# Kernel tuning notes

Hardware: AMD Instinct MI355X
Metric: run time of the kernel (lower is better)

## Reference

```python
import jax, jax.numpy as jnp
import numpy as np

DIN = 512      # input feature dim (din)
HEADS = 8
DHEAD = 64
DIM = HEADS * DHEAD  # 512
NTOT = 12288   # total nodes across all graphs
NBATCH = 32    # number of graphs
NMAX = 512     # padded max nodes per graph (<= pf_threshold ~562 -> softmax branch)
EPS = 1e-5


def setup_inputs() -> dict:
    key = jax.random.key(0)
    ks = jax.random.split(key, 7)
    z = jax.random.normal(ks[0], (NTOT, DIN), jnp.float32)
    src = jnp.sort(jax.random.randint(ks[1], (NTOT,), 0, NBATCH)).astype(jnp.int32)
    w_scale = 1.0 / np.sqrt(DIN)
    Wq = jax.random.normal(ks[2], (DIN, DIM), jnp.float32) * w_scale
    Wk = jax.random.normal(ks[3], (DIN, DIM), jnp.float32) * w_scale
    Wv = jax.random.normal(ks[4], (DIN, DIM), jnp.float32) * w_scale
    Wo = jax.random.normal(ks[5], (DIM, DIM), jnp.float32) * w_scale
    bo = jnp.zeros((DIM,), jnp.float32)
    ln_gamma = jnp.ones((DIN,), jnp.float32)
    ln_beta = jnp.zeros((DIN,), jnp.float32)
    return {"z": z, "src": src, "ln_gamma": ln_gamma, "ln_beta": ln_beta,
            "Wq": Wq, "Wk": Wk, "Wv": Wv, "Wo": Wo, "bo": bo,
            "n_max": NMAX, "n_batch": NBATCH}


def reference(z, src, ln_gamma, ln_beta, Wq, Wk, Wv, Wo, bo, n_max, n_batch):
    # --- LayerNorm(din) ---
    mu = jnp.mean(z, axis=-1, keepdims=True)
    var = jnp.mean(jnp.square(z - mu), axis=-1, keepdims=True)
    zn = (z - mu) * jax.lax.rsqrt(var + EPS) * ln_gamma + ln_beta

    # --- to_dense_batch(zn, src): src is sorted graph-id per node ---
    ntot = z.shape[0]
    counts = jnp.bincount(src, length=n_batch)                    # [B]
    starts = jnp.concatenate([jnp.zeros((1,), counts.dtype), jnp.cumsum(counts)[:-1]])
    pos = jnp.arange(ntot) - starts[src]                          # position within graph
    x = jnp.zeros((n_batch, n_max, DIN), zn.dtype).at[src, pos].set(zn)   # [B,N,din]
    mask = jnp.zeros((n_batch, n_max), bool).at[src, pos].set(True)       # [B,N]

    # --- q/k/v projections, split heads: b n (h d) -> b h n d ---
    def heads(t):
        return t.reshape(n_batch, n_max, HEADS, DHEAD).transpose(0, 2, 1, 3)
    q = heads(x @ Wq)
    k = heads(x @ Wk)
    v = heads(x @ Wv)

    # --- manual masked softmax attention (N <= pf_threshold branch) ---
    s = jnp.einsum('bhmd,bhnd->bhmn', q, k)
    s = jnp.where(mask[:, None, None, :], s, -jnp.inf)
    a = jax.nn.softmax(s * (DHEAD ** -0.5), axis=-1)
    o = jnp.einsum('bhmn,bhnd->bhmd', a, v)

    # --- merge heads, gather valid rows (out[mask]), output projection ---
    o = o.transpose(0, 2, 1, 3).reshape(n_batch, n_max, DIM)
    h = o[src, pos] @ Wo + bo                                     # [Ntot, DIM]
    return h
```

## Files before the change

### kernel.cpp

```cpp
#include <hip/hip_runtime.h>
#include <hip/hip_bf16.h>
#include <math.h>

#define DIN 512
#define DIM 512
#define NHEADS 8
#define DHEAD 64
#define NB 32
#define NPAD 512
#define NPTOT (NB * NPAD)

typedef __attribute__((ext_vector_type(8))) short bf16x8;
typedef __attribute__((ext_vector_type(8))) unsigned short u16x8;
typedef __attribute__((ext_vector_type(4))) float f32x4;

typedef __attribute__((address_space(3))) unsigned int lds_u32;
typedef __attribute__((address_space(1))) const unsigned int g_u32;

__device__ __forceinline__ void gll16(const unsigned short* g, unsigned short* l) {
  __builtin_amdgcn_global_load_lds((g_u32*)g, (lds_u32*)l, 16, 0, 0);
}

__device__ inline unsigned short f2bf(float x) {
  unsigned int u = __float_as_uint(x);
  unsigned int r = (u + 0x7FFFu + ((u >> 16) & 1u)) >> 16;
  return (unsigned short)r;
}

#define BAR()   __builtin_amdgcn_s_barrier()
#define LGKM0() asm volatile("s_waitcnt lgkmcnt(0)" ::: "memory")
#define LGKM8() asm volatile("s_waitcnt lgkmcnt(8)" ::: "memory")
#define VMCNT(n) asm volatile("s_waitcnt vmcnt(" #n ")" ::: "memory")

__global__ __launch_bounds__(256) void prep_kernel(const float* __restrict__ z,
                                                   const float* __restrict__ gamma,
                                                   const float* __restrict__ beta,
                                                   const int* __restrict__ src,
                                                   const float* __restrict__ Wq,
                                                   const float* __restrict__ Wk,
                                                   const float* __restrict__ Wv,
                                                   const float* __restrict__ Wo,
                                                   unsigned short* __restrict__ zn,
                                                   int* __restrict__ starts,
                                                   int* __restrict__ dstrow,
                                                   unsigned short* __restrict__ WtQKV,
                                                   unsigned short* __restrict__ WtO,
                                                   int ntot) {
  __shared__ float tile[32][33];
  int b = blockIdx.x;
  int nln = ntot >> 2;
  int nmap = (ntot + 255) >> 8;
  if (b < nln) {
    int wave = b * 4 + (threadIdx.x >> 6);
    int lane = threadIdx.x & 63;
    const float* row = z + (size_t)wave * DIN;
    float4 a = ((const float4*)row)[lane];
    float4 bb = ((const float4*)row)[64 + lane];
    float s  = a.x + a.y + a.z + a.w + bb.x + bb.y + bb.z + bb.w;
    float sq = a.x*a.x + a.y*a.y + a.z*a.z + a.w*a.w
             + bb.x*bb.x + bb.y*bb.y + bb.z*bb.z + bb.w*bb.w;
#pragma unroll
    for (int off = 32; off; off >>= 1) {
      s  += __shfl_xor(s, off);
      sq += __shfl_xor(sq, off);
    }
    float mu  = s * (1.0f / DIN);
    float var = sq * (1.0f / DIN) - mu * mu;
    float r   = rsqrtf(var + 1e-5f);
    float4 g0 = ((const float4*)gamma)[lane];
    float4 g1 = ((const float4*)gamma)[64 + lane];
    float4 b0 = ((const float4*)beta)[lane];
    float4 b1 = ((const float4*)beta)[64 + lane];
    ushort4 o0, o1;
    o0.x = f2bf((a.x - mu) * r * g0.x + b0.x);
    o0.y = f2bf((a.y - mu) * r * g0.y + b0.y);
    o0.z = f2bf((a.z - mu) * r * g0.z + b0.z);
    o0.w = f2bf((a.w - mu) * r * g0.w + b0.w);
    o1.x = f2bf((bb.x - mu) * r * g1.x + b1.x);
    o1.y = f2bf((bb.y - mu) * r * g1.y + b1.y);
    o1.z = f2bf((bb.z - mu) * r * g1.z + b1.z);
    o1.w = f2bf((bb.w - mu) * r * g1.w + b1.w);
    ((ushort4*)(zn + (size_t)wave * DIN))[lane] = o0;
    ((ushort4*)(zn + (size_t)wave * DIN))[64 + lane] = o1;
  } else if (b < nln + nmap) {
    int bid = b - nln;
    if (bid == 0 && threadIdx.x <= NB) {
      int gg = threadIdx.x;
      int lo = 0, hi = ntot;
      while (lo < hi) { int mid = (lo + hi) >> 1; if (src[mid] < gg) lo = mid + 1; else hi = mid; }
      starts[gg] = lo;
    }
    int i = bid * 256 + threadIdx.x;
    if (i < ntot) {
      int gg = src[i];
      int lo = 0, hi = ntot;
      while (lo < hi) { int mid = (lo + hi) >> 1; if (src[mid] < gg) lo = mid + 1; else hi = mid; }
      dstrow[i] = gg * NPAD + (i - lo);
    }
  } else {
    int idx = b - nln - nmap;
    int zz = idx >> 8;
    int rem = idx & 255;
    const float* W; unsigned short* Wt;
    if (zz == 0)      { W = Wq; Wt = WtQKV; }
    else if (zz == 1) { W = Wk; Wt = WtQKV + (size_t)512 * DIN; }
    else if (zz == 2) { W = Wv; Wt = WtQKV + (size_t)1024 * DIN; }
    else              { W = Wo; Wt = WtO; }
    int k0 = (rem & 15) * 32;
    int n0 = (rem >> 4) * 32;
    int tx = threadIdx.x & 31;
    int ty = threadIdx.x >> 5;
#pragma unroll
    for (int i = 0; i < 4; i++)
      tile[ty + i * 8][tx] = W[(size_t)(k0 + ty + i * 8) * DIM + n0 + tx];
    __syncthreads();
#pragma unroll
    for (int i = 0; i < 4; i++)
      Wt[(size_t)(n0 + ty + i * 8) * DIN + k0 + tx] = f2bf(tile[tx][ty + i * 8]);
  }
}

__global__ __launch_bounds__(512) void gemm_qkv_8ph(const unsigned short* __restrict__ A,
                                                    const unsigned short* __restrict__ Bt,
                                                    const int* __restrict__ remap,
                                                    unsigned short* __restrict__ C) {
  __shared__ unsigned short smem[65536];
  const int tid = threadIdx.x;
  const int lane = tid & 63, wv = tid >> 6;
  const int wr = wv >> 2, wc = wv & 3;
  const int col16 = lane & 15, quad = lane >> 4;
  const int m0 = blockIdx.x * 256, n0 = blockIdx.y * 256;

  f32x4 acc[2][2][4][2];
#pragma unroll
  for (int qa = 0; qa < 2; ++qa)
#pragma unroll
    for (int qb = 0; qb < 2; ++qb)
#pragma unroll
      for (int mt = 0; mt < 4; ++mt)
#pragma unroll
        for (int nt = 0; nt < 2; ++nt) acc[qa][qb][mt][nt] = (f32x4){0.f, 0.f, 0.f, 0.f};

  bf16x8 af[4][2], bf[2][2];

  auto stage = [&](int par, int w, const unsigned short* G, int row0, int kt) {
    unsigned short* base = smem + par * 32768 + w * 8192;
#pragma unroll
    for (int i = 0; i < 2; ++i) {
      int c1k = wv * 2 + i;
      int r = row0 + c1k * 8 + (lane >> 3);
      int p = (lane & 7) ^ (lane >> 3);
      gll16(G + (size_t)r * 512 + kt * 64 + p * 8, base + c1k * 512);
    }
  };
  auto loadA = [&](int par, int half) {
    const unsigned short* base = smem + par * 32768 + half * 8192;
#pragma unroll
    for (int mt = 0; mt < 4; ++mt) {
      int r = wr * 64 + mt * 16 + col16;
      int sw = r & 7;
      af[mt][0] = *(const bf16x8*)&base[r * 64 + ((quad ^ sw) * 8)];
      af[mt][1] = *(const bf16x8*)&base[r * 64 + (((quad + 4) ^ sw) * 8)];
    }
  };
  auto loadB = [&](int par, int half) {
    const unsigned short* base = smem + par * 32768 + (2 + half) * 8192;
#pragma unroll
    for (int nt = 0; nt < 2; ++nt) {
      int r = wc * 32 + nt * 16 + col16;
      int sw = r & 7;
      bf[nt][0] = *(const bf16x8*)&base[r * 64 + ((quad ^ sw) * 8)];
      bf[nt][1] = *(const bf16x8*)&base[r * 64 + (((quad + 4) ^ sw) * 8)];
    }
  };
  auto mfmaQ = [&](int qa, int qb) {
    __builtin_amdgcn_s_setprio(1);
#pragma unroll
    for (int mt = 0; mt < 4; ++mt)
#pragma unroll
      for (int nt = 0; nt < 2; ++nt) {
        acc[qa][qb][mt][nt] =
            __builtin_amdgcn_mfma_f32_16x16x32_bf16(af[mt][0], bf[nt][0], acc[qa][qb][mt][nt], 0, 0, 0);
        acc[qa][qb][mt][nt] =
            __builtin_amdgcn_mfma_f32_16x16x32_bf16(af[mt][1], bf[nt][1], acc[qa][qb][mt][nt], 0, 0, 0);
      }
    __builtin_amdgcn_s_setprio(0);
  };

  stage(0, 0, A,  m0,       0);
  stage(0, 3, Bt, n0 + 128, 0);
  stage(0, 1, A,  m0 + 128, 0);
  stage(0, 2, Bt, n0,       0);
  stage(1, 0, A,  m0,       1);
  stage(1, 3, Bt, n0 + 128, 1);
  VMCNT(4);
  BAR();

#pragma unroll
  for (int i = 0; i < 4; ++i) {
    const int t1 = 2 * i + 1, t2 = 2 * i + 2, t3 = 2 * i + 3;
    const bool more = (i < 3);
    loadA(0, 0); loadB(0, 0);
    stage(1, 1, A, m0 + 128, t1);
    LGKM8();
    BAR(); LGKM0();
    mfmaQ(0, 0);
    BAR();
    loadB(0, 1);
    stage(1, 2, Bt, n0, t1);
    BAR(); LGKM0();
    mfmaQ(0, 1);
    BAR();
    loadA(0, 1);
    if (more) stage(0, 0, A, m0, t2);
    BAR(); LGKM0();
    mfmaQ(1, 1);
    BAR();
    loadB(0, 0);
    if (more) stage(0, 3, Bt, n0 + 128, t2);
    BAR(); LGKM0();
    mfmaQ(1, 0);
    if (more) { VMCNT(4); } else { VMCNT(0); }
    BAR();
    loadA(1, 0); loadB(1, 0);
    if (more) stage(0, 1, A, m0 + 128, t2);
    LGKM8();
    BAR(); LGKM0();
    mfmaQ(0, 0);
    BAR();
    loadB(1, 1);
    if (more) stage(0, 2, Bt, n0, t2);
    BAR(); LGKM0();
    mfmaQ(0, 1);
    BAR();
    loadA(1, 1);
    if (more) stage(1, 0, A, m0, t3);
    BAR(); LGKM0();
    mfmaQ(1, 1);
    BAR();
    loadB(1, 0);
    if (more) stage(1, 3, Bt, n0 + 128, t3);
    BAR(); LGKM0();
    mfmaQ(1, 0);
    if (more) VMCNT(4);
    BAR();
  }

#pragma unroll
  for (int qa = 0; qa < 2; ++qa)
#pragma unroll
    for (int qb = 0; qb < 2; ++qb)
#pragma unroll
      for (int mt = 0; mt < 4; ++mt)
#pragma unroll
        for (int nt = 0; nt < 2; ++nt)
#pragma unroll
          for (int r = 0; r < 4; ++r) {
            int row = qa * 128 + wr * 64 + mt * 16 + quad * 4 + r;
            int c   = qb * 128 + wc * 32 + nt * 16 + col16;
            smem[row * 256 + (((c >> 3) ^ (row & 31)) * 8) + (c & 7)] = f2bf(acc[qa][qb][mt][nt][r]);
          }
  __syncthreads();
#pragma unroll
  for (int pass = 0; pass < 16; ++pass) {
    int row = pass * 16 + (tid >> 5);
    int ch  = tid & 31;
    u16x8 v = *(const u16x8*)&smem[row * 256 + ((ch ^ (row & 31)) * 8)];
    int drow = remap[m0 + row];
    *(u16x8*)(C + (size_t)drow * 1536 + n0 + ch * 8) = v;
  }
}

template <int NCOLS, bool BIAS, bool OUT_F32, bool REMAP>
__global__ __launch_bounds__(256) void gemm_staged(const unsigned short* __restrict__ A,
                                                   const unsigned short* __restrict__ Bt,
                                                   const float* __restrict__ bias,
                                                   const int* __restrict__ remap,
                                                   unsigned short* __restrict__ Cbf,
                                                   float* __restrict__ Cf) {
  __shared__ unsigned short smem[16384];
  int tid = threadIdx.x, lane = tid & 63, wv = tid >> 6;
  int col = lane & 15, quad = lane >> 4;
  int m0 = blockIdx.x * 128, n0 = blockIdx.y * 128;
  int msub = (wv & 1) * 64, nsub = (wv >> 1) * 64;

  int srow = lane >> 2;
  int cswz = (((lane & 3) ^ ((lane >> 3) & 3))) * 8;

  f32x4 acc[4][4];
#pragma unroll
  for (int i = 0; i < 4; i++)
#pragma unroll
    for (int j = 0; j < 4; j++) acc[i][j] = (f32x4){0.f, 0.f, 0.f, 0.f};

  auto stage = [&](int ks, int nb) {
    const unsigned short* Ab = A  + (size_t)m0 * DIN + ks * 32;
    const unsigned short* Bb = Bt + (size_t)n0 * DIN + ks * 32;
#pragma unroll
    for (int i = 0; i < 2; i++) {
      int t = wv * 2 + i;
      gll16(Ab + (size_t)(t * 16 + srow) * DIN + cswz, smem + nb * 4096 + t * 512);
      gll16(Bb + (size_t)(t * 16 + srow) * DIN + cswz, smem + 8192 + nb * 4096 + t * 512);
    }
  };

  stage(0, 0);
#pragma unroll 2
  for (int ks = 0; ks < 16; ks++) {
    int cur = ks & 1;
    __syncthreads();
    if (ks + 1 < 16) stage(ks + 1, 1 - cur);
    bf16x8 af[4], bfr[4];
#pragma unroll
    for (int mt = 0; mt < 4; mt++) {
      int row = msub + mt * 16 + col;
      af[mt] = *(const bf16x8*)&smem[cur * 4096 + row * 32 + ((quad ^ ((row >> 1) & 3)) * 8)];
    }
#pragma unroll
    for (int nt = 0; nt < 4; nt++) {
      int row = nsub + nt * 16 + col;
      bfr[nt] = *(const bf16x8*)&smem[8192 + cur * 4096 + row * 32 + ((quad ^ ((row >> 1) & 3)) * 8)];
    }
#pragma unroll
    for (int mt = 0; mt < 4; mt++)
#pragma unroll
      for (int nt = 0; nt < 4; nt++)
        acc[mt][nt] = __builtin_amdgcn_mfma_f32_16x16x32_bf16(af[mt], bfr[nt], acc[mt][nt], 0, 0, 0);
  }

  if (!OUT_F32) {
    __syncthreads();
#pragma unroll
    for (int mt = 0; mt < 4; mt++)
#pragma unroll
      for (int r = 0; r < 4; r++) {
        int row = msub + mt * 16 + quad * 4 + r;
#pragma unroll
        for (int nt = 0; nt < 4; nt++) {
          int c = nsub + nt * 16 + col;
          float v = acc[mt][nt][r] + (BIAS ? bias[n0 + c] : 0.f);
          smem[row * 128 + (((c >> 3) ^ (quad << 1)) * 8) + (c & 7)] = f2bf(v);
        }
      }
    __syncthreads();
#pragma unroll
    for (int pass = 0; pass < 8; pass++) {
      int row = pass * 16 + (tid >> 4);
      int sw  = ((row >> 2) & 3) << 1;
      int ch  = tid & 15;
      u16x8 vv = *(const u16x8*)&smem[row * 128 + ((ch ^ sw) * 8)];
      int drow = REMAP ? remap[m0 + row] : (m0 + row);
      *(u16x8*)(Cbf + (size_t)drow * NCOLS + n0 + ch * 8) = vv;
    }
  } else {
#pragma unroll
    for (int mt = 0; mt < 4; mt++) {
#pragma unroll
      for (int r = 0; r < 4; r++) {
        int mrow = m0 + msub + mt * 16 + quad * 4 + r;
#pragma unroll
        for (int nt = 0; nt < 4; nt++) {
          int ncol = n0 + nsub + nt * 16 + col;
          Cf[(size_t)mrow * NCOLS + ncol] = acc[mt][nt][r] + (BIAS ? bias[ncol] : 0.f);
        }
      }
    }
  }
}

__global__ __launch_bounds__(256, 3) void fattn_kernel(const unsigned short* __restrict__ qkvp,
                                                       const int* __restrict__ starts,
                                                       unsigned short* __restrict__ obuf) {
  __shared__ unsigned short Kbuf[2][64 * 64];
  __shared__ unsigned short Vbuf[2][64 * 64];
  __shared__ unsigned short Plds[4][32 * 64];
  int g = blockIdx.x, h = blockIdx.y, qt = blockIdx.z;
  int st = starts[g];
  int n  = starts[g + 1] - st;
  int q0b = qt * 128;
  if (q0b >= n) return;
  int tid = threadIdx.x, lane = tid & 63, wv = tid >> 6;
  int col = lane & 15, quad = lane >> 4;
  int q0 = q0b + wv * 32;
  bool active = q0 < n;
  int ntiles = (n + 63) >> 6;

  bf16x8 qf[2][2];
  if (active) {
#pragma unroll
    for (int a = 0; a < 2; a++) {
      const unsigned short* qp = qkvp + (size_t)(g * NPAD + q0 + a * 16 + col) * 1536 + h * 64 + quad * 8;
      qf[a][0] = *(const bf16x8*)(qp);
      qf[a][1] = *(const bf16x8*)(qp + 32);
    }
  }

  int srow = tid >> 2;
  int sc   = (tid & 3) * 2;
  int woff0 = srow * 64 + ((sc ^ (srow & 7)) * 8);
  int woff1 = srow * 64 + (((sc + 1) ^ (srow & 7)) * 8);
  u16x8 kreg0, kreg1, vreg0, vreg1;
  auto loadregs = [&](int kt) {
    const unsigned short* kp = qkvp + (size_t)(g * NPAD + kt + srow) * 1536 + 512 + h * 64 + sc * 8;
    kreg0 = *(const u16x8*)(kp);
    kreg1 = *(const u16x8*)(kp + 8);
    vreg0 = *(const u16x8*)(kp + 512);
    vreg1 = *(const u16x8*)(kp + 520);
  };
  auto writelds = [&](int bsel) {
    *(u16x8*)&Kbuf[bsel][woff0] = kreg0;
    *(u16x8*)&Kbuf[bsel][woff1] = kreg1;
#pragma unroll
    for (int i = 0; i < 8; i++) {
      int c0 = sc * 8 + i;
      int c1 = sc * 8 + 8 + i;
      Vbuf[bsel][c0 * 64 + (((srow >> 3) ^ ((c0 >> 4) << 1) ^ (c0 & 7)) * 8) + (srow & 7)] = vreg0[i];
      Vbuf[bsel][c1 * 64 + (((srow >> 3) ^ ((c1 >> 4) << 1) ^ (c1 & 7)) * 8) + (srow & 7)] = vreg1[i];
    }
  };

  bf16x8 onesv;
#pragma unroll
  for (int i = 0; i < 8; i++) onesv[i] = (short)0x3F80;

  f32x4 oa[2][4];
  f32x4 lacc[2];
#pragma unroll
  for (int a = 0; a < 2; a++) {
    lacc[a] = (f32x4){0.f, 0.f, 0.f, 0.f};
#pragma unroll
    for (int i = 0; i < 4; i++) oa[a][i] = (f32x4){0.f, 0.f, 0.f, 0.f};
  }

  loadregs(0);
  writelds(0);
  __syncthreads();

  for (int t = 0; t < ntiles; t++) {
    int cur = t & 1;
    if (t + 1 < ntiles) loadregs((t + 1) * 64);
    if (active) {
      f32x4 s[2][4];
#pragma unroll
      for (int a = 0; a < 2; a++)
#pragma unroll
        for (int j = 0; j < 4; j++) s[a][j] = (f32x4){0.f, 0.f, 0.f, 0.f};
#pragma unroll
      for (int j = 0; j < 4; j++) {
        int R = j * 16 + col;
        bf16x8 kf0 = *(const bf16x8*)&Kbuf[cur][R * 64 + ((quad ^ (R & 7)) * 8)];
        bf16x8 kf1 = *(const bf16x8*)&Kbuf[cur][R * 64 + (((4 + quad) ^ (R & 7)) * 8)];
        s[0][j] = __builtin_amdgcn_mfma_f32_16x16x32_bf16(qf[0][0], kf0, s[0][j], 0, 0, 0);
        s[0][j] = __builtin_amdgcn_mfma_f32_16x16x32_bf16(qf[0][1], kf1, s[0][j], 0, 0, 0);
        s[1][j] = __builtin_amdgcn_mfma_f32_16x16x32_bf16(qf[1][0], kf0, s[1][j], 0, 0, 0);
        s[1][j] = __builtin_amdgcn_mfma_f32_16x16x32_bf16(qf[1][1], kf1, s[1][j], 0, 0, 0);
      }
      int kt = t * 64;
#pragma unroll
      for (int j = 0; j < 4; j++) {
        bool valid = (kt + j * 16 + col) < n;
#pragma unroll
        for (int a = 0; a < 2; a++)
#pragma unroll
          for (int r = 0; r < 4; r++)
            s[a][j][r] = valid ? __expf(s[a][j][r] * 0.125f) : 0.f;
      }
#pragma unroll
      for (int a = 0; a < 2; a++)
#pragma unroll
        for (int r = 0; r < 4; r++) {
          int R = a * 16 + quad * 4 + r;
#pragma unroll
          for (int j = 0; j < 4; j++) {
            int chunk = j * 2 + (col >> 3);
            Plds[wv][R * 64 + ((chunk ^ (R & 7)) * 8) + (col & 7)] = f2bf(s[a][j][r]);
          }
        }
      __builtin_amdgcn_fence(__ATOMIC_ACQ_REL, "workgroup");
      bf16x8 pf[2][2];
#pragma unroll
      for (int a = 0; a < 2; a++) {
        int R = a * 16 + col;
        pf[a][0] = *(const bf16x8*)&Plds[wv][R * 64 + ((quad ^ (col & 7)) * 8)];
        pf[a][1] = *(const bf16x8*)&Plds[wv][R * 64 + (((4 + quad) ^ (col & 7)) * 8)];
      }
#pragma unroll
      for (int dt = 0; dt < 4; dt++) {
        int R = dt * 16 + col;
        int gR = ((R >> 4) << 1) ^ (R & 7);
        bf16x8 vf0 = *(const bf16x8*)&Vbuf[cur][R * 64 + ((quad ^ gR) * 8)];
        bf16x8 vf1 = *(const bf16x8*)&Vbuf[cur][R * 64 + (((quad + 4) ^ gR) * 8)];
        oa[0][dt] = __builtin_amdgcn_mfma_f32_16x16x32_bf16(pf[0][0], vf0, oa[0][dt], 0, 0, 0);
        oa[0][dt] = __builtin_amdgcn_mfma_f32_16x16x32_bf16(pf[0][1], vf1, oa[0][dt], 0, 0, 0);
        oa[1][dt] = __builtin_amdgcn_mfma_f32_16x16x32_bf16(pf[1][0], vf0, oa[1][dt], 0, 0, 0);
        oa[1][dt] = __builtin_amdgcn_mfma_f32_16x16x32_bf16(pf[1][1], vf1, oa[1][dt], 0, 0, 0);
      }
      lacc[0] = __builtin_amdgcn_mfma_f32_16x16x32_bf16(pf[0][0], onesv, lacc[0], 0, 0, 0);
      lacc[0] = __builtin_amdgcn_mfma_f32_16x16x32_bf16(pf[0][1], onesv, lacc[0], 0, 0, 0);
      lacc[1] = __builtin_amdgcn_mfma_f32_16x16x32_bf16(pf[1][0], onesv, lacc[1], 0, 0, 0);
      lacc[1] = __builtin_amdgcn_mfma_f32_16x16x32_bf16(pf[1][1], onesv, lacc[1], 0, 0, 0);
    }
    if (t + 1 < ntiles) writelds(1 - cur);
    __syncthreads();
  }

  if (active) {
#pragma unroll
    for (int a = 0; a < 2; a++)
#pragma unroll
      for (int r = 0; r < 4; r++) {
        int q = q0 + a * 16 + quad * 4 + r;
        if (q < n) {
          float inv = 1.0f / lacc[a][r];
          unsigned short* op = obuf + (size_t)(st + q) * DIM + h * 64 + col;
          op[0]  = f2bf(oa[a][0][r] * inv);
          op[16] = f2bf(oa[a][1][r] * inv);
          op[32] = f2bf(oa[a][2][r] * inv);
          op[48] = f2bf(oa[a][3][r] * inv);
        }
      }
  }
}

extern "C" void kernel_launch(void* const* d_in, const int* in_sizes, int n_in,
                              void* d_out, int out_size, void* d_ws, size_t ws_size,
                              hipStream_t stream) {
  const float* z     = (const float*)d_in[0];
  const int*   src   = (const int*)d_in[1];
  const float* gamma = (const float*)d_in[2];
  const float* beta  = (const float*)d_in[3];
  const float* Wq    = (const float*)d_in[4];
  const float* Wk    = (const float*)d_in[5];
  const float* Wv    = (const float*)d_in[6];
  const float* Wo    = (const float*)d_in[7];
  const float* bo    = (const float*)d_in[8];
  int ntot = in_sizes[0] / DIN;
  float* out = (float*)d_out;

  char* ws = (char*)d_ws;
  size_t off = 0;
  unsigned short* zn    = (unsigned short*)(ws + off); off += (size_t)ntot * DIN * 2;
  unsigned short* qkvp  = (unsigned short*)(ws + off); off += (size_t)NPTOT * 1536 * 2;
  unsigned short* obuf  = (unsigned short*)(ws + off); off += (size_t)ntot * DIM * 2;
  unsigned short* WtQKV = (unsigned short*)(ws + off); off += (size_t)1536 * DIN * 2;
  unsigned short* WtO   = (unsigned short*)(ws + off); off += (size_t)DIM * DIN * 2;
  int* starts           = (int*)(ws + off);            off += 64 * 4;
  int* dstrow           = (int*)(ws + off);

  int nln = ntot >> 2;
  int nmap = (ntot + 255) >> 8;
  prep_kernel<<<nln + nmap + 1024, 256, 0, stream>>>(z, gamma, beta, src, Wq, Wk, Wv, Wo,
                                                     zn, starts, dstrow, WtQKV, WtO, ntot);

  gemm_qkv_8ph<<<dim3(ntot / 256, 1536 / 256), 512, 0, stream>>>(zn, WtQKV, dstrow, qkvp);

  fattn_kernel<<<dim3(NB, NHEADS, 4), 256, 0, stream>>>(qkvp, starts, obuf);

  gemm_staged<512, true, true, false>
      <<<dim3(ntot / 128, 4), 256, 0, stream>>>(obuf, WtO, bo, nullptr, nullptr, out);
}
```

Before: 179.9 us.

## Retile QKV GEMM to 192x384 blocks with reworked staging schedule

Measured after the change: 178.5 us. Within noise of the previous version (-0.8%).

```diff
diff --git a/kernel.cpp b/kernel.cpp
--- a/kernel.cpp
+++ b/kernel.cpp
@@ -124,125 +124,131 @@
                                                     const unsigned short* __restrict__ Bt,
                                                     const int* __restrict__ remap,
                                                     unsigned short* __restrict__ C) {
-  __shared__ unsigned short smem[65536];
+  __shared__ unsigned short smem[75264];
   const int tid = threadIdx.x;
   const int lane = tid & 63, wv = tid >> 6;
   const int wr = wv >> 2, wc = wv & 3;
   const int col16 = lane & 15, quad = lane >> 4;
-  const int m0 = blockIdx.x * 256, n0 = blockIdx.y * 256;
-
-  f32x4 acc[2][2][4][2];
+  const int m0 = (blockIdx.x >> 2) * 192, n0 = (blockIdx.x & 3) * 384;
+
+  f32x4 acc[2][2][3][3];
 #pragma unroll
   for (int qa = 0; qa < 2; ++qa)
 #pragma unroll
     for (int qb = 0; qb < 2; ++qb)
 #pragma unroll
-      for (int mt = 0; mt < 4; ++mt)
-#pragma unroll
-        for (int nt = 0; nt < 2; ++nt) acc[qa][qb][mt][nt] = (f32x4){0.f, 0.f, 0.f, 0.f};
-
-  bf16x8 af[4][2], bf[2][2];
-
-  auto stage = [&](int par, int w, const unsigned short* G, int row0, int kt) {
-    unsigned short* base = smem + par * 32768 + w * 8192;
-#pragma unroll
-    for (int i = 0; i < 2; ++i) {
-      int c1k = wv * 2 + i;
-      int r = row0 + c1k * 8 + (lane >> 3);
+      for (int mt = 0; mt < 3; ++mt)
+#pragma unroll
+        for (int nt = 0; nt < 3; ++nt) acc[qa][qb][mt][nt] = (f32x4){0.f, 0.f, 0.f, 0.f};
+
+  bf16x8 af[3][2], bb[3][2];
+
+  auto stageA = [&](int par, int kt) {
+    unsigned short* base = smem + par * 36864;
+#pragma unroll
+    for (int i = 0; i < 3; ++i) {
+      int c = wv * 3 + i;
+      int r = m0 + c * 8 + (lane >> 3);
       int p = (lane & 7) ^ (lane >> 3);
-      gll16(G + (size_t)r * 512 + kt * 64 + p * 8, base + c1k * 512);
-    }
-  };
-  auto loadA = [&](int par, int half) {
-    const unsigned short* base = smem + par * 32768 + half * 8192;
-#pragma unroll
-    for (int mt = 0; mt < 4; ++mt) {
-      int r = wr * 64 + mt * 16 + col16;
+      gll16(A + (size_t)r * 512 + kt * 64 + p * 8, base + c * 512);
+    }
+  };
+  auto stageBh = [&](int par, int h, int kt) {
+    unsigned short* base = smem + par * 36864 + 12288 + h * 12288;
+#pragma unroll
+    for (int i = 0; i < 3; ++i) {
+      int c = wv * 3 + i;
+      int r = n0 + h * 192 + c * 8 + (lane >> 3);
+      int p = (lane & 7) ^ (lane >> 3);
+      gll16(Bt + (size_t)r * 512 + kt * 64 + p * 8, base + c * 512);
+    }
+  };
+  auto loadA = [&](int par, int qa) {
+    const unsigned short* base = smem + par * 36864;
+#pragma unroll
+    for (int mt = 0; mt < 3; ++mt) {
+      int r = wr * 96 + qa * 48 + mt * 16 + col16;
       int sw = r & 7;
       af[mt][0] = *(const bf16x8*)&base[r * 64 + ((quad ^ sw) * 8)];
       af[mt][1] = *(const bf16x8*)&base[r * 64 + (((quad + 4) ^ sw) * 8)];
     }
   };
-  auto loadB = [&](int par, int half) {
-    const unsigned short* base = smem + par * 32768 + (2 + half) * 8192;
-#pragma unroll
-    for (int nt = 0; nt < 2; ++nt) {
-      int r = wc * 32 + nt * 16 + col16;
+  auto loadB = [&](int par, int qb) {
+    const unsigned short* base = smem + par * 36864 + 12288;
+#pragma unroll
+    for (int nt = 0; nt < 3; ++nt) {
+      int r = wc * 96 + qb * 48 + nt * 16 + col16;
       int sw = r & 7;
-      bf[nt][0] = *(const bf16x8*)&base[r * 64 + ((quad ^ sw) * 8)];
-      bf[nt][1] = *(const bf16x8*)&base[r * 64 + (((quad + 4) ^ sw) * 8)];
+      bb[nt][0] = *(const bf16x8*)&base[r * 64 + ((quad ^ sw) * 8)];
+      bb[nt][1] = *(const bf16x8*)&base[r * 64 + (((quad + 4) ^ sw) * 8)];
     }
   };
   auto mfmaQ = [&](int qa, int qb) {
     __builtin_amdgcn_s_setprio(1);
 #pragma unroll
-    for (int mt = 0; mt < 4; ++mt)
-#pragma unroll
-      for (int nt = 0; nt < 2; ++nt) {
+    for (int mt = 0; mt < 3; ++mt)
+#pragma unroll
+      for (int nt = 0; nt < 3; ++nt) {
         acc[qa][qb][mt][nt] =
-            __builtin_amdgcn_mfma_f32_16x16x32_bf16(af[mt][0], bf[nt][0], acc[qa][qb][mt][nt], 0, 0, 0);
+            __builtin_amdgcn_mfma_f32_16x16x32_bf16(af[mt][0], bb[nt][0], acc[qa][qb][mt][nt], 0, 0, 0);
         acc[qa][qb][mt][nt] =
-            __builtin_amdgcn_mfma_f32_16x16x32_bf16(af[mt][1], bf[nt][1], acc[qa][qb][mt][nt], 0, 0, 0);
+            __builtin_amdgcn_mfma_f32_16x16x32_bf16(af[mt][1], bb[nt][1], acc[qa][qb][mt][nt], 0, 0, 0);
       }
     __builtin_amdgcn_s_setprio(0);
   };
 
-  stage(0, 0, A,  m0,       0);
-  stage(0, 3, Bt, n0 + 128, 0);
-  stage(0, 1, A,  m0 + 128, 0);
-  stage(0, 2, Bt, n0,       0);
-  stage(1, 0, A,  m0,       1);
-  stage(1, 3, Bt, n0 + 128, 1);
-  VMCNT(4);
+  stageA(0, 0);
+  stageBh(0, 0, 0);
+  stageBh(0, 1, 0);
+  stageA(1, 1);
+  VMCNT(3);
   BAR();
 
-#pragma unroll
+#pragma unroll 1
   for (int i = 0; i < 4; ++i) {
-    const int t1 = 2 * i + 1, t2 = 2 * i + 2, t3 = 2 * i + 3;
+    const int t_o = 2 * i + 1, t_e2 = 2 * i + 2, t_o2 = 2 * i + 3;
     const bool more = (i < 3);
     loadA(0, 0); loadB(0, 0);
-    stage(1, 1, A, m0 + 128, t1);
+    stageBh(1, 0, t_o);
     LGKM8();
     BAR(); LGKM0();
     mfmaQ(0, 0);
     BAR();
     loadB(0, 1);
-    stage(1, 2, Bt, n0, t1);
+    stageBh(1, 1, t_o);
     BAR(); LGKM0();
     mfmaQ(0, 1);
     BAR();
     loadA(0, 1);
-    if (more) stage(0, 0, A, m0, t2);
     BAR(); LGKM0();
     mfmaQ(1, 1);
     BAR();
     loadB(0, 0);
-    if (more) stage(0, 3, Bt, n0 + 128, t2);
+    if (more) stageA(0, t_e2);
     BAR(); LGKM0();
     mfmaQ(1, 0);
-    if (more) { VMCNT(4); } else { VMCNT(0); }
+    if (more) { VMCNT(3); } else { VMCNT(0); }
     BAR();
     loadA(1, 0); loadB(1, 0);
-    if (more) stage(0, 1, A, m0 + 128, t2);
+    if (more) stageBh(0, 0, t_e2);
     LGKM8();
     BAR(); LGKM0();
     mfmaQ(0, 0);
     BAR();
     loadB(1, 1);
-    if (more) stage(0, 2, Bt, n0, t2);
+    if (more) stageBh(0, 1, t_e2);
     BAR(); LGKM0();
     mfmaQ(0, 1);
     BAR();
     loadA(1, 1);
-    if (more) stage(1, 0, A, m0, t3);
     BAR(); LGKM0();
     mfmaQ(1, 1);
     BAR();
     loadB(1, 0);
-    if (more) stage(1, 3, Bt, n0 + 128, t3);
+    if (more) stageA(1, t_o2);
     BAR(); LGKM0();
     mfmaQ(1, 0);
-    if (more) VMCNT(4);
+    if (more) { VMCNT(3); } else { VMCNT(0); }
     BAR();
   }
 
@@ -251,21 +257,22 @@
 #pragma unroll
     for (int qb = 0; qb < 2; ++qb)
 #pragma unroll
-      for (int mt = 0; mt < 4; ++mt)
-#pragma unroll
-        for (int nt = 0; nt < 2; ++nt)
+      for (int mt = 0; mt < 3; ++mt)
+#pragma unroll
+        for (int nt = 0; nt < 3; ++nt)
 #pragma unroll
           for (int r = 0; r < 4; ++r) {
-            int row = qa * 128 + wr * 64 + mt * 16 + quad * 4 + r;
-            int c   = qb * 128 + wc * 32 + nt * 16 + col16;
-            smem[row * 256 + (((c >> 3) ^ (row & 31)) * 8) + (c & 7)] = f2bf(acc[qa][qb][mt][nt][r]);
+            int row = wr * 96 + qa * 48 + mt * 16 + quad * 4 + r;
+            int c   = wc * 96 + qb * 48 + nt * 16 + col16;
+            smem[row * 392 + c] = f2bf(acc[qa][qb][mt][nt][r]);
           }
   __syncthreads();
 #pragma unroll
-  for (int pass = 0; pass < 16; ++pass) {
-    int row = pass * 16 + (tid >> 5);
-    int ch  = tid & 31;
-    u16x8 v = *(const u16x8*)&smem[row * 256 + ((ch ^ (row & 31)) * 8)];
+  for (int pass = 0; pass < 18; ++pass) {
+    int idx = pass * 512 + tid;
+    int row = (int)(((unsigned)idx * 43691u) >> 21);
+    int ch  = idx - row * 48;
+    u16x8 v = *(const u16x8*)&smem[row * 392 + ch * 8];
     int drow = remap[m0 + row];
     *(u16x8*)(C + (size_t)drow * 1536 + n0 + ch * 8) = v;
   }
@@ -552,7 +559,7 @@
   prep_kernel<<<nln + nmap + 1024, 256, 0, stream>>>(z, gamma, beta, src, Wq, Wk, Wv, Wo,
                                                      zn, starts, dstrow, WtQKV, WtO, ntot);
 
-  gemm_qkv_8ph<<<dim3(ntot / 256, 1536 / 256), 512, 0, stream>>>(zn, WtQKV, dstrow, qkvp);
+  gemm_qkv_8ph<<<(ntot / 192) * 4, 512, 0, stream>>>(zn, WtQKV, dstrow, qkvp);
 
   fattn_kernel<<<dim3(NB, NHEADS, 4), 256, 0, stream>>>(qkvp, starts, obuf);
 
```
